# Kernel optimization log

Hardware: AMD Instinct MI355X
Metric: run time of the kernel (lower is better)

The kernel has to match this reference:

```python
import jax, jax.numpy as jnp
import numpy as np

N_NODES = 50000
N_EDGES = 800000
IN_DIM = 128
HID = 128
NUM_CLASSES = 2


def setup_inputs() -> dict:
    key = jax.random.key(0)
    ks = jax.random.split(key, 16)
    inp = {
        "adj_row": jax.random.randint(ks[0], (N_EDGES,), 0, N_NODES),
        "adj_col": jax.random.randint(ks[1], (N_EDGES,), 0, N_NODES),
        "adj_vals": jax.random.uniform(ks[2], (N_EDGES,), dtype=jnp.float32),
        "input_feature": jax.random.normal(ks[3], (N_NODES, IN_DIM), dtype=jnp.float32),
        "graph_indicator": jax.random.randint(ks[4], (N_NODES,), 0, 64),
        # GCN layer params (kaiming-uniform-ish init; zeros bias like the torch module)
        "W1": jax.random.uniform(ks[5], (IN_DIM, HID), jnp.float32, -1, 1) * np.sqrt(6.0 / IN_DIM),
        "b1": jnp.zeros((HID,), jnp.float32),
        "W2": jax.random.uniform(ks[6], (HID, HID), jnp.float32, -1, 1) * np.sqrt(6.0 / HID),
        "b2": jnp.zeros((HID,), jnp.float32),
        "W3": jax.random.uniform(ks[7], (HID, HID), jnp.float32, -1, 1) * np.sqrt(6.0 / HID),
        "b3": jnp.zeros((HID,), jnp.float32),
        # fc params (torch.nn.Linear default init range)
        "fcW1": jax.random.uniform(ks[8], (3 * HID, HID), jnp.float32, -1, 1) / np.sqrt(3 * HID),
        "fcb1": jax.random.uniform(ks[9], (HID,), jnp.float32, -1, 1) / np.sqrt(3 * HID),
        "fcW2": jax.random.uniform(ks[10], (HID, HID // 2), jnp.float32, -1, 1) / np.sqrt(HID),
        "fcb2": jax.random.uniform(ks[11], (HID // 2,), jnp.float32, -1, 1) / np.sqrt(HID),
        "fcW3": jax.random.uniform(ks[12], (HID // 2, NUM_CLASSES), jnp.float32, -1, 1) / np.sqrt(HID // 2),
        "fcb3": jax.random.uniform(ks[13], (NUM_CLASSES,), jnp.float32, -1, 1) / np.sqrt(HID // 2),
    }
    return inp


def _gcn_layer(row, col, vals, x, W, b, n_nodes):
    # support = X @ W  -> dense GEMM
    support = x @ W
    # sparse.mm(A, support): out[i] = sum_{e: row[e]=i} vals[e] * support[col[e]]
    msgs = support[col] * vals[:, None]  # [E, D] gather + scale
    agg = jax.ops.segment_sum(msgs, row, num_segments=n_nodes)
    return agg + b


def reference(adj_row, adj_col, adj_vals, input_feature, graph_indicator,
              W1, b1, W2, b2, W3, b3, fcW1, fcb1, fcW2, fcb2, fcW3, fcb3):
    n = input_feature.shape[0]
    g1 = jax.nn.relu(_gcn_layer(adj_row, adj_col, adj_vals, input_feature, W1, b1, n))
    g2 = jax.nn.relu(_gcn_layer(adj_row, adj_col, adj_vals, g1, W2, b2, n))
    g3 = jax.nn.relu(_gcn_layer(adj_row, adj_col, adj_vals, g2, W3, b3, n))
    feat = jnp.concatenate([g1, g2, g3], axis=1)  # [N, 3*HID]
    h = jax.nn.relu(feat @ fcW1 + fcb1)
    h = jax.nn.relu(h @ fcW2 + fcb2)
    logits = h @ fcW3 + fcb3
    return logits
```

## Files before the change

kernel.cpp:

```cpp
#include <hip/hip_runtime.h>
#include <hip/hip_bf16.h>

#define N_NODES 50000
#define N_EDGES 800000
#define NBK 391
#define BCAP 2560

static inline int cdiv(int a, int b) { return (a + b - 1) / b; }

typedef __attribute__((ext_vector_type(8))) short short8;
typedef __attribute__((ext_vector_type(4))) float f32x4;

__device__ __forceinline__ float b2f(unsigned short u) {
    union { unsigned int i; float f; } c;
    c.i = ((unsigned int)u) << 16;
    return c.f;
}
__device__ __forceinline__ unsigned short f2bb(float f) {
    __hip_bfloat16 h = __float2bfloat16(f);
    return *(unsigned short*)&h;
}


__global__ __launch_bounds__(256)
void binA_kernel(const int* __restrict__ row, const int* __restrict__ col,
                 const float* __restrict__ vals, int* __restrict__ bcursor,
                 int2* __restrict__ tmp, int E) {
    __shared__ int hist[NBK];
    __shared__ int base[NBK];
    const int CH = 4096;
    int e0 = blockIdx.x * CH;
    for (int i = threadIdx.x; i < NBK; i += 256) hist[i] = 0;
    __syncthreads();
    for (int i = threadIdx.x; i < CH; i += 256) {
        int e = e0 + i;
        if (e < E) atomicAdd(&hist[row[e] >> 7], 1);
    }
    __syncthreads();
    for (int i = threadIdx.x; i < NBK; i += 256) {
        int c = hist[i];
        base[i] = (c > 0) ? atomicAdd(&bcursor[i], c) : 0;
        hist[i] = 0;
    }
    __syncthreads();
    for (int i = threadIdx.x; i < CH; i += 256) {
        int e = e0 + i;
        if (e < E) {
            int r = row[e];
            int b = r >> 7;
            int rk = atomicAdd(&hist[b], 1);
            tmp[base[b] + rk] = make_int2(((r & 127) << 16) | col[e],
                                          __float_as_int(vals[e]));
        }
    }
}

__global__ __launch_bounds__(512)
void bscan_kernel(const int* __restrict__ bcursor, int* __restrict__ bbase) {
    __shared__ int s[512];
    int t = threadIdx.x;
    int v = (t < NBK) ? (bcursor[t] - t * BCAP) : 0;
    s[t] = v;
    __syncthreads();
    for (int off = 1; off < 512; off <<= 1) {
        int u = (t >= off) ? s[t - off] : 0;
        __syncthreads();
        s[t] += u;
        __syncthreads();
    }
    if (t < NBK) bbase[t] = s[t] - v;
    if (t == NBK - 1) bbase[NBK] = s[t];
}

__global__ __launch_bounds__(256)
void binB_kernel(const int2* __restrict__ tmp, const int* __restrict__ bcursor,
                 const int* __restrict__ bbase, int* __restrict__ row_ptr,
                 int2* __restrict__ epack, int N) {
    int b = blockIdx.x;
    int r0 = b << 7;
    int nr = N - r0; if (nr > 128) nr = 128;
    __shared__ int cnt[128];
    __shared__ int cur[128];
    int t = threadIdx.x;
    if (t < 128) cnt[t] = 0;
    __syncthreads();
    int slab = b * BCAP;
    int send = bcursor[b];
    int obase = bbase[b];
    for (int i = slab + t; i < send; i += 256)
        atomicAdd(&cnt[tmp[i].x >> 16], 1);
    __syncthreads();
    if (t < 128) cur[t] = cnt[t];
    __syncthreads();
    for (int off = 1; off < 128; off <<= 1) {
        int u = (t >= off && t < 128) ? cur[t - off] : 0;
        __syncthreads();
        if (t < 128) cur[t] += u;
        __syncthreads();
    }
    if (t < 128) {
        int ex = cur[t] - cnt[t];
        int pos = obase + ex;
        cur[t] = pos;
        if (t < nr) row_ptr[r0 + t] = pos;
    }
    if (b == NBK - 1 && t == 128) row_ptr[N] = bbase[NBK];
    __syncthreads();
    for (int i = slab + t; i < send; i += 256) {
        int2 v = tmp[i];
        int rl = v.x >> 16;
        int c = v.x & 0xffff;
        int pos = atomicAdd(&cur[rl], 1);
        epack[pos] = make_int2(c, v.y);
    }
}


__device__ __forceinline__ void pack_one(const float* __restrict__ W,
                                         __hip_bfloat16* __restrict__ out,
                                         int K, int N, int t) {
    int lane = t & 63;
    int kc = (t >> 6) % (K / 32);
    int nt = (t >> 6) / (K / 32);
    int kbase = kc * 32 + (lane >> 4) * 8;
    int col = nt * 16 + (lane & 15);
    __hip_bfloat16* dst = out + (size_t)t * 8;
#pragma unroll
    for (int j = 0; j < 8; ++j)
        dst[j] = __float2bfloat16(W[(size_t)(kbase + j) * N + col]);
}

__global__ __launch_bounds__(256)
void prep_kernel(const float* __restrict__ W1, const float* __restrict__ W2,
                 const float* __restrict__ W3, const float* __restrict__ fcW1,
                 const float* __restrict__ fcW2,
                 __hip_bfloat16* __restrict__ pW1, __hip_bfloat16* __restrict__ pW2,
                 __hip_bfloat16* __restrict__ pW3, __hip_bfloat16* __restrict__ pfcW1,
                 __hip_bfloat16* __restrict__ pfcW2, int* __restrict__ bcursor) {
    int b = blockIdx.x;
    if (b < 8)       pack_one(W1,  pW1,  128, 128, b * 256 + threadIdx.x);
    else if (b < 16) pack_one(W2,  pW2,  128, 128, (b - 8) * 256 + threadIdx.x);
    else if (b < 24) pack_one(W3,  pW3,  128, 128, (b - 16) * 256 + threadIdx.x);
    else if (b < 48) pack_one(fcW1, pfcW1, 384, 128, (b - 24) * 256 + threadIdx.x);
    else if (b < 52) pack_one(fcW2, pfcW2, 128, 64, (b - 48) * 256 + threadIdx.x);
    else {
        int t = (b - 52) * 256 + threadIdx.x;
        if (t < NBK) bcursor[t] = t * BCAP;
    }
}

template <int KTOT, int N, bool RELU, bool BIAS, bool AFP32>
__global__ __launch_bounds__(256, 3)
void mfma_gemm(const void* __restrict__ Aptr, int lda,
               const __hip_bfloat16* __restrict__ pW,
               const float* __restrict__ bias,
               __hip_bfloat16* __restrict__ C, int ldc, int M) {
    constexpr int NS = (N == 128) ? 2 : 1;
    constexpr int KC = KTOT / 32;
    __shared__ unsigned short As[64][136];
    const int tid = threadIdx.x;
    const int wave = tid >> 6;
    const int lane = tid & 63;
    const int ln15 = lane & 15;
    const int quad = lane >> 4;
    const int m0 = blockIdx.x * 64;
    const int ntw = wave * NS;

    f32x4 acc[4][NS];
#pragma unroll
    for (int s = 0; s < 4; ++s)
#pragma unroll
        for (int h = 0; h < NS; ++h) acc[s][h] = (f32x4){0.f, 0.f, 0.f, 0.f};

    for (int kb = 0; kb < KTOT / 128; ++kb) {
#pragma unroll
        for (int i = 0; i < 4; ++i) {
            int idx = tid + i * 256;
            int r = idx >> 4;
            int c8 = (idx & 15) * 8;
            if constexpr (AFP32) {
                const float* A = (const float*)Aptr;
                uint4 pk = {0, 0, 0, 0};
                if (m0 + r < M) {
                    const float* src = &A[(size_t)(m0 + r) * lda + kb * 128 + c8];
                    float4 a = *(const float4*)src;
                    float4 bq = *(const float4*)(src + 4);
                    pk.x = f2bb(a.x) | ((unsigned int)f2bb(a.y) << 16);
                    pk.y = f2bb(a.z) | ((unsigned int)f2bb(a.w) << 16);
                    pk.z = f2bb(bq.x) | ((unsigned int)f2bb(bq.y) << 16);
                    pk.w = f2bb(bq.z) | ((unsigned int)f2bb(bq.w) << 16);
                }
                *(uint4*)&As[r][c8] = pk;
            } else {
                const __hip_bfloat16* A = (const __hip_bfloat16*)Aptr;
                uint4 v = *(const uint4*)&A[(size_t)(m0 + r) * lda + kb * 128 + c8];
                *(uint4*)&As[r][c8] = v;
            }
        }
        __syncthreads();
#pragma unroll
        for (int kc = 0; kc < 4; ++kc) {
            short8 af[4];
#pragma unroll
            for (int s = 0; s < 4; ++s)
                af[s] = *(const short8*)&As[s * 16 + ln15][kc * 32 + quad * 8];
            short8 bf[NS];
#pragma unroll
            for (int h = 0; h < NS; ++h) {
                int kcg = kb * 4 + kc;
                bf[h] = *(const short8*)&pW[((size_t)((ntw + h) * KC + kcg) * 64 + lane) * 8];
            }
#pragma unroll
            for (int s = 0; s < 4; ++s)
#pragma unroll
                for (int h = 0; h < NS; ++h)
                    acc[s][h] = __builtin_amdgcn_mfma_f32_16x16x32_bf16(
                        af[s], bf[h], acc[s][h], 0, 0, 0);
        }
        __syncthreads();
    }

#pragma unroll
    for (int s = 0; s < 4; ++s) {
#pragma unroll
        for (int h = 0; h < NS; ++h) {
            int col = (ntw + h) * 16 + ln15;
            float bv = BIAS ? bias[col] : 0.f;
#pragma unroll
            for (int r = 0; r < 4; ++r) {
                int row = m0 + s * 16 + quad * 4 + r;
                if (row < M) {
                    float v = acc[s][h][r] + bv;
                    if (RELU) v = fmaxf(v, 0.f);
                    C[(size_t)row * ldc + col] = __float2bfloat16(v);
                }
            }
        }
    }
}

__global__ __launch_bounds__(256, 3)
void fc123_kernel(const __hip_bfloat16* __restrict__ featb,
                  const __hip_bfloat16* __restrict__ pfcW1,
                  const float* __restrict__ fcb1,
                  const __hip_bfloat16* __restrict__ pfcW2,
                  const float* __restrict__ fcb2,
                  const float* __restrict__ fcW3, const float* __restrict__ fcb3,
                  float* __restrict__ out, int M) {
    __shared__ unsigned short As[64][136];
    __shared__ float w3s[128];
    __shared__ float b3s[2];
    const int tid = threadIdx.x;
    const int wave = tid >> 6;
    const int lane = tid & 63;
    const int ln15 = lane & 15;
    const int quad = lane >> 4;
    const int m0 = blockIdx.x * 64;
    if (tid < 128) w3s[tid] = fcW3[tid];
    if (tid < 2) b3s[tid] = fcb3[tid];

    f32x4 acc[4][2];
#pragma unroll
    for (int s = 0; s < 4; ++s)
#pragma unroll
        for (int h = 0; h < 2; ++h) acc[s][h] = (f32x4){0.f, 0.f, 0.f, 0.f};
    for (int kb = 0; kb < 3; ++kb) {
#pragma unroll
        for (int i = 0; i < 4; ++i) {
            int idx = tid + i * 256;
            int r = idx >> 4;
            int c8 = (idx & 15) * 8;
            uint4 v = *(const uint4*)&featb[(size_t)(m0 + r) * 384 + kb * 128 + c8];
            *(uint4*)&As[r][c8] = v;
        }
        __syncthreads();
#pragma unroll
        for (int kc = 0; kc < 4; ++kc) {
            short8 af[4];
#pragma unroll
            for (int s = 0; s < 4; ++s)
                af[s] = *(const short8*)&As[s * 16 + ln15][kc * 32 + quad * 8];
            short8 bf[2];
#pragma unroll
            for (int h = 0; h < 2; ++h) {
                int kcg = kb * 4 + kc;
                bf[h] = *(const short8*)&pfcW1[((size_t)((wave * 2 + h) * 12 + kcg) * 64 + lane) * 8];
            }
#pragma unroll
            for (int s = 0; s < 4; ++s)
#pragma unroll
                for (int h = 0; h < 2; ++h)
                    acc[s][h] = __builtin_amdgcn_mfma_f32_16x16x32_bf16(
                        af[s], bf[h], acc[s][h], 0, 0, 0);
        }
        __syncthreads();
    }
#pragma unroll
    for (int s = 0; s < 4; ++s)
#pragma unroll
        for (int h = 0; h < 2; ++h) {
            int col = (wave * 2 + h) * 16 + ln15;
            float bv = fcb1[col];
#pragma unroll
            for (int r = 0; r < 4; ++r) {
                int row = s * 16 + quad * 4 + r;
                As[row][col] = f2bb(fmaxf(acc[s][h][r] + bv, 0.f));
            }
        }
    __syncthreads();

    f32x4 acc2[4];
#pragma unroll
    for (int s = 0; s < 4; ++s) acc2[s] = (f32x4){0.f, 0.f, 0.f, 0.f};
#pragma unroll
    for (int kc = 0; kc < 4; ++kc) {
        short8 af[4];
#pragma unroll
        for (int s = 0; s < 4; ++s)
            af[s] = *(const short8*)&As[s * 16 + ln15][kc * 32 + quad * 8];
        short8 bfw = *(const short8*)&pfcW2[((size_t)(wave * 4 + kc) * 64 + lane) * 8];
#pragma unroll
        for (int s = 0; s < 4; ++s)
            acc2[s] = __builtin_amdgcn_mfma_f32_16x16x32_bf16(af[s], bfw, acc2[s], 0, 0, 0);
    }
    __syncthreads();
    {
        int col2 = wave * 16 + ln15;
        float bv = fcb2[col2];
#pragma unroll
        for (int s = 0; s < 4; ++s)
#pragma unroll
            for (int r = 0; r < 4; ++r) {
                int row = s * 16 + quad * 4 + r;
                As[row][col2] = f2bb(fmaxf(acc2[s][r] + bv, 0.f));
            }
    }
    __syncthreads();

    if (tid < 128) {
        int row = tid >> 1, cls = tid & 1;
        int grow = m0 + row;
        if (grow < M) {
            float a = b3s[cls];
#pragma unroll
            for (int k = 0; k < 64; ++k)
                a += b2f(As[row][k]) * w3s[k * 2 + cls];
            out[(size_t)grow * 2 + cls] = a;
        }
    }
}

__global__ __launch_bounds__(256)
void spmm_kernel(const int* __restrict__ row_ptr, const int2* __restrict__ epack,
                 const __hip_bfloat16* __restrict__ support,
                 const float* __restrict__ bias, __hip_bfloat16* __restrict__ out,
                 int ldo, int n) {
    int wv = threadIdx.x >> 6;
    int l = threadIdx.x & 63;
    int node = blockIdx.x * 4 + wv;
    if (node >= n) return;
    int start = row_ptr[node], end = row_ptr[node + 1];
    float ax = 0.f, ay = 0.f;
    int p = start;
    for (; p + 4 <= end; p += 4) {
        int2 e0 = epack[p], e1 = epack[p + 1], e2 = epack[p + 2], e3 = epack[p + 3];
        ushort2 u0 = *(const ushort2*)&support[(size_t)e0.x * 128 + l * 2];
        ushort2 u1 = *(const ushort2*)&support[(size_t)e1.x * 128 + l * 2];
        ushort2 u2 = *(const ushort2*)&support[(size_t)e2.x * 128 + l * 2];
        ushort2 u3 = *(const ushort2*)&support[(size_t)e3.x * 128 + l * 2];
        float v0 = __int_as_float(e0.y), v1 = __int_as_float(e1.y);
        float v2 = __int_as_float(e2.y), v3 = __int_as_float(e3.y);
        ax += v0 * b2f(u0.x) + v1 * b2f(u1.x) + v2 * b2f(u2.x) + v3 * b2f(u3.x);
        ay += v0 * b2f(u0.y) + v1 * b2f(u1.y) + v2 * b2f(u2.y) + v3 * b2f(u3.y);
    }
    for (; p < end; ++p) {
        int2 e0 = epack[p];
        float v0 = __int_as_float(e0.y);
        ushort2 u0 = *(const ushort2*)&support[(size_t)e0.x * 128 + l * 2];
        ax += v0 * b2f(u0.x);
        ay += v0 * b2f(u0.y);
    }
    ushort2 ov;
    ov.x = f2bb(fmaxf(ax + bias[l * 2 + 0], 0.f));
    ov.y = f2bb(fmaxf(ay + bias[l * 2 + 1], 0.f));
    *(ushort2*)&out[(size_t)node * ldo + l * 2] = ov;
}

extern "C" void kernel_launch(void* const* d_in, const int* in_sizes, int n_in,
                              void* d_out, int out_size, void* d_ws, size_t ws_size,
                              hipStream_t stream) {
    const int*   adj_row  = (const int*)d_in[0];
    const int*   adj_col  = (const int*)d_in[1];
    const float* adj_vals = (const float*)d_in[2];
    const float* x        = (const float*)d_in[3];
    const float* W1   = (const float*)d_in[5];
    const float* b1   = (const float*)d_in[6];
    const float* W2   = (const float*)d_in[7];
    const float* b2   = (const float*)d_in[8];
    const float* W3   = (const float*)d_in[9];
    const float* b3   = (const float*)d_in[10];
    const float* fcW1 = (const float*)d_in[11];
    const float* fcb1 = (const float*)d_in[12];
    const float* fcW2 = (const float*)d_in[13];
    const float* fcb2 = (const float*)d_in[14];
    const float* fcW3 = (const float*)d_in[15];
    const float* fcb3 = (const float*)d_in[16];
    float* out = (float*)d_out;

    const int N = N_NODES, E = N_EDGES;
    const int Mpad = 50048;

    char* p = (char*)d_ws;
    auto alloc = [&](size_t bytes) {
        char* q = p;
        p += (bytes + 255) & ~(size_t)255;
        return q;
    };
    __hip_bfloat16* featb    = (__hip_bfloat16*)alloc((size_t)Mpad * 384 * 2);
    __hip_bfloat16* supportb = (__hip_bfloat16*)alloc((size_t)Mpad * 128 * 2);
    __hip_bfloat16* pW1   = (__hip_bfloat16*)alloc(16384 * 2);
    __hip_bfloat16* pW2   = (__hip_bfloat16*)alloc(16384 * 2);
    __hip_bfloat16* pW3   = (__hip_bfloat16*)alloc(16384 * 2);
    __hip_bfloat16* pfcW1 = (__hip_bfloat16*)alloc(49152 * 2);
    __hip_bfloat16* pfcW2 = (__hip_bfloat16*)alloc(8192 * 2);
    int*   row_ptr   = (int*)alloc((size_t)(N + 1) * 4);
    int*   bbase     = (int*)alloc((size_t)(NBK + 1) * 4);
    int*   bcursor   = (int*)alloc((size_t)NBK * 4);
    int2*  epack     = (int2*)alloc((size_t)E * 8);
    int2*  tmp = (int2*)(featb + (size_t)Mpad * 384 - (size_t)NBK * BCAP * 4);

    prep_kernel<<<54, 256, 0, stream>>>(W1, W2, W3, fcW1, fcW2,
                                        pW1, pW2, pW3, pfcW1, pfcW2, bcursor);
    binA_kernel<<<cdiv(E, 4096), 256, 0, stream>>>(adj_row, adj_col, adj_vals,
                                                   bcursor, tmp, E);
    bscan_kernel<<<1, 512, 0, stream>>>(bcursor, bbase);
    binB_kernel<<<NBK, 256, 0, stream>>>(tmp, bcursor, bbase, row_ptr, epack, N);

    const int gemmGrid = cdiv(N, 64);
    const int spmmGrid = cdiv(N, 4);

    mfma_gemm<128, 128, false, false, true><<<gemmGrid, 256, 0, stream>>>(
        x, 128, pW1, nullptr, supportb, 128, N);
    spmm_kernel<<<spmmGrid, 256, 0, stream>>>(row_ptr, epack, supportb, b1,
                                              featb + 0, 384, N);
    mfma_gemm<128, 128, false, false, false><<<gemmGrid, 256, 0, stream>>>(
        featb + 0, 384, pW2, nullptr, supportb, 128, N);
    spmm_kernel<<<spmmGrid, 256, 0, stream>>>(row_ptr, epack, supportb, b2,
                                              featb + 128, 384, N);
    mfma_gemm<128, 128, false, false, false><<<gemmGrid, 256, 0, stream>>>(
        featb + 128, 384, pW3, nullptr, supportb, 128, N);
    spmm_kernel<<<spmmGrid, 256, 0, stream>>>(row_ptr, epack, supportb, b3,
                                              featb + 256, 384, N);

    fc123_kernel<<<gemmGrid, 256, 0, stream>>>(featb, pfcW1, fcb1, pfcW2, fcb2,
                                               fcW3, fcb3, out, N);
}
```

Baseline: 302.6 us.

## Fuse SpMM aggregation with following GEMM and final FC into combined kernels

Each sparse aggregation is now done inside a 64-node block, written straight to shared memory and immediately multiplied by the next layer weight, so the separate GEMM kernels and their reloads of the feature matrix go away. The last layer's aggregation feeds fcW1 directly, so g3 is never written to global memory and the feature buffer shrinks to 256 columns. Support buffers are double-buffered and the edge list is read with nontemporal loads. The cost is that one block now aggregates 64 nodes with four waves instead of many small blocks, which lowers gather parallelism and latency hiding per block.

```diff
diff --git a/kernel.cpp b/kernel.cpp
--- a/kernel.cpp
+++ b/kernel.cpp
@@ -149,14 +149,10 @@
     }
 }
 
-template <int KTOT, int N, bool RELU, bool BIAS, bool AFP32>
 __global__ __launch_bounds__(256, 3)
-void mfma_gemm(const void* __restrict__ Aptr, int lda,
-               const __hip_bfloat16* __restrict__ pW,
-               const float* __restrict__ bias,
-               __hip_bfloat16* __restrict__ C, int ldc, int M) {
-    constexpr int NS = (N == 128) ? 2 : 1;
-    constexpr int KC = KTOT / 32;
+void gemm1_kernel(const float* __restrict__ A,
+                  const __hip_bfloat16* __restrict__ pW,
+                  __hip_bfloat16* __restrict__ C, int M) {
     __shared__ unsigned short As[64][136];
     const int tid = threadIdx.x;
     const int wave = tid >> 6;
@@ -164,90 +160,179 @@
     const int ln15 = lane & 15;
     const int quad = lane >> 4;
     const int m0 = blockIdx.x * 64;
-    const int ntw = wave * NS;
-
-    f32x4 acc[4][NS];
+    const int ntw = wave * 2;
+
+    f32x4 acc[4][2];
 #pragma unroll
     for (int s = 0; s < 4; ++s)
 #pragma unroll
-        for (int h = 0; h < NS; ++h) acc[s][h] = (f32x4){0.f, 0.f, 0.f, 0.f};
-
-    for (int kb = 0; kb < KTOT / 128; ++kb) {
-#pragma unroll
-        for (int i = 0; i < 4; ++i) {
-            int idx = tid + i * 256;
-            int r = idx >> 4;
-            int c8 = (idx & 15) * 8;
-            if constexpr (AFP32) {
-                const float* A = (const float*)Aptr;
-                uint4 pk = {0, 0, 0, 0};
-                if (m0 + r < M) {
-                    const float* src = &A[(size_t)(m0 + r) * lda + kb * 128 + c8];
-                    float4 a = *(const float4*)src;
-                    float4 bq = *(const float4*)(src + 4);
-                    pk.x = f2bb(a.x) | ((unsigned int)f2bb(a.y) << 16);
-                    pk.y = f2bb(a.z) | ((unsigned int)f2bb(a.w) << 16);
-                    pk.z = f2bb(bq.x) | ((unsigned int)f2bb(bq.y) << 16);
-                    pk.w = f2bb(bq.z) | ((unsigned int)f2bb(bq.w) << 16);
-                }
-                *(uint4*)&As[r][c8] = pk;
-            } else {
-                const __hip_bfloat16* A = (const __hip_bfloat16*)Aptr;
-                uint4 v = *(const uint4*)&A[(size_t)(m0 + r) * lda + kb * 128 + c8];
-                *(uint4*)&As[r][c8] = v;
-            }
-        }
-        __syncthreads();
-#pragma unroll
-        for (int kc = 0; kc < 4; ++kc) {
-            short8 af[4];
-#pragma unroll
-            for (int s = 0; s < 4; ++s)
-                af[s] = *(const short8*)&As[s * 16 + ln15][kc * 32 + quad * 8];
-            short8 bf[NS];
-#pragma unroll
-            for (int h = 0; h < NS; ++h) {
-                int kcg = kb * 4 + kc;
-                bf[h] = *(const short8*)&pW[((size_t)((ntw + h) * KC + kcg) * 64 + lane) * 8];
-            }
-#pragma unroll
-            for (int s = 0; s < 4; ++s)
-#pragma unroll
-                for (int h = 0; h < NS; ++h)
-                    acc[s][h] = __builtin_amdgcn_mfma_f32_16x16x32_bf16(
-                        af[s], bf[h], acc[s][h], 0, 0, 0);
-        }
-        __syncthreads();
-    }
-
-#pragma unroll
-    for (int s = 0; s < 4; ++s) {
-#pragma unroll
-        for (int h = 0; h < NS; ++h) {
+        for (int h = 0; h < 2; ++h) acc[s][h] = (f32x4){0.f, 0.f, 0.f, 0.f};
+
+#pragma unroll
+    for (int i = 0; i < 4; ++i) {
+        int idx = tid + i * 256;
+        int r = idx >> 4;
+        int c8 = (idx & 15) * 8;
+        uint4 pk = {0, 0, 0, 0};
+        if (m0 + r < M) {
+            const float* src = &A[(size_t)(m0 + r) * 128 + c8];
+            float4 a = *(const float4*)src;
+            float4 bq = *(const float4*)(src + 4);
+            pk.x = f2bb(a.x) | ((unsigned int)f2bb(a.y) << 16);
+            pk.y = f2bb(a.z) | ((unsigned int)f2bb(a.w) << 16);
+            pk.z = f2bb(bq.x) | ((unsigned int)f2bb(bq.y) << 16);
+            pk.w = f2bb(bq.z) | ((unsigned int)f2bb(bq.w) << 16);
+        }
+        *(uint4*)&As[r][c8] = pk;
+    }
+    __syncthreads();
+#pragma unroll
+    for (int kc = 0; kc < 4; ++kc) {
+        short8 af[4];
+#pragma unroll
+        for (int s = 0; s < 4; ++s)
+            af[s] = *(const short8*)&As[s * 16 + ln15][kc * 32 + quad * 8];
+        short8 bf[2];
+#pragma unroll
+        for (int h = 0; h < 2; ++h)
+            bf[h] = *(const short8*)&pW[((size_t)((ntw + h) * 4 + kc) * 64 + lane) * 8];
+#pragma unroll
+        for (int s = 0; s < 4; ++s)
+#pragma unroll
+            for (int h = 0; h < 2; ++h)
+                acc[s][h] = __builtin_amdgcn_mfma_f32_16x16x32_bf16(
+                    af[s], bf[h], acc[s][h], 0, 0, 0);
+    }
+
+#pragma unroll
+    for (int s = 0; s < 4; ++s)
+#pragma unroll
+        for (int h = 0; h < 2; ++h) {
             int col = (ntw + h) * 16 + ln15;
-            float bv = BIAS ? bias[col] : 0.f;
 #pragma unroll
             for (int r = 0; r < 4; ++r) {
                 int row = m0 + s * 16 + quad * 4 + r;
-                if (row < M) {
-                    float v = acc[s][h][r] + bv;
-                    if (RELU) v = fmaxf(v, 0.f);
-                    C[(size_t)row * ldc + col] = __float2bfloat16(v);
-                }
+                if (row < M)
+                    C[(size_t)row * 128 + col] = __float2bfloat16(acc[s][h][r]);
             }
         }
+}
+
+__device__ __forceinline__ void agg_node(const int* __restrict__ row_ptr,
+                                         const long long* __restrict__ ep,
+                                         const __hip_bfloat16* __restrict__ support,
+                                         int node, int lane, float& ax, float& ay) {
+    int pstart = row_ptr[node], pend = row_ptr[node + 1];
+    int p = pstart;
+    for (; p + 4 <= pend; p += 4) {
+        long long v0 = __builtin_nontemporal_load(&ep[p]);
+        long long v1 = __builtin_nontemporal_load(&ep[p + 1]);
+        long long v2 = __builtin_nontemporal_load(&ep[p + 2]);
+        long long v3 = __builtin_nontemporal_load(&ep[p + 3]);
+        ushort2 u0 = *(const ushort2*)&support[(size_t)(unsigned int)(v0 & 0xffffffff) * 128 + lane * 2];
+        ushort2 u1 = *(const ushort2*)&support[(size_t)(unsigned int)(v1 & 0xffffffff) * 128 + lane * 2];
+        ushort2 u2 = *(const ushort2*)&support[(size_t)(unsigned int)(v2 & 0xffffffff) * 128 + lane * 2];
+        ushort2 u3 = *(const ushort2*)&support[(size_t)(unsigned int)(v3 & 0xffffffff) * 128 + lane * 2];
+        float f0 = __int_as_float((int)(v0 >> 32));
+        float f1 = __int_as_float((int)(v1 >> 32));
+        float f2 = __int_as_float((int)(v2 >> 32));
+        float f3 = __int_as_float((int)(v3 >> 32));
+        ax += f0 * b2f(u0.x) + f1 * b2f(u1.x) + f2 * b2f(u2.x) + f3 * b2f(u3.x);
+        ay += f0 * b2f(u0.y) + f1 * b2f(u1.y) + f2 * b2f(u2.y) + f3 * b2f(u3.y);
+    }
+    for (; p < pend; ++p) {
+        long long v0 = __builtin_nontemporal_load(&ep[p]);
+        ushort2 u0 = *(const ushort2*)&support[(size_t)(unsigned int)(v0 & 0xffffffff) * 128 + lane * 2];
+        float f0 = __int_as_float((int)(v0 >> 32));
+        ax += f0 * b2f(u0.x);
+        ay += f0 * b2f(u0.y);
     }
 }
 
 __global__ __launch_bounds__(256, 3)
-void fc123_kernel(const __hip_bfloat16* __restrict__ featb,
-                  const __hip_bfloat16* __restrict__ pfcW1,
-                  const float* __restrict__ fcb1,
-                  const __hip_bfloat16* __restrict__ pfcW2,
-                  const float* __restrict__ fcb2,
-                  const float* __restrict__ fcW3, const float* __restrict__ fcb3,
-                  float* __restrict__ out, int M) {
+void spmm_gemm_kernel(const int* __restrict__ row_ptr, const int2* __restrict__ epack,
+                      const __hip_bfloat16* __restrict__ support_in,
+                      const float* __restrict__ bias,
+                      __hip_bfloat16* __restrict__ featb_slice,
+                      const __hip_bfloat16* __restrict__ pW,
+                      __hip_bfloat16* __restrict__ support_out, int M) {
     __shared__ unsigned short As[64][136];
+    const int tid = threadIdx.x;
+    const int wave = tid >> 6;
+    const int lane = tid & 63;
+    const int ln15 = lane & 15;
+    const int quad = lane >> 4;
+    const int m0 = blockIdx.x * 64;
+    const long long* ep = (const long long*)epack;
+    const float b0 = bias[lane * 2], b1v = bias[lane * 2 + 1];
+
+    for (int i = 0; i < 16; ++i) {
+        int r = wave * 16 + i;
+        int node = m0 + r;
+        float ax = 0.f, ay = 0.f;
+        unsigned int packed = 0;
+        if (node < M) {
+            agg_node(row_ptr, ep, support_in, node, lane, ax, ay);
+            ax = fmaxf(ax + b0, 0.f);
+            ay = fmaxf(ay + b1v, 0.f);
+            packed = (unsigned int)f2bb(ax) | ((unsigned int)f2bb(ay) << 16);
+            __builtin_nontemporal_store(packed,
+                (unsigned int*)&featb_slice[(size_t)node * 256 + lane * 2]);
+        }
+        *(unsigned int*)&As[r][lane * 2] = packed;
+    }
+    __syncthreads();
+
+    f32x4 acc[4][2];
+#pragma unroll
+    for (int s = 0; s < 4; ++s)
+#pragma unroll
+        for (int h = 0; h < 2; ++h) acc[s][h] = (f32x4){0.f, 0.f, 0.f, 0.f};
+#pragma unroll
+    for (int kc = 0; kc < 4; ++kc) {
+        short8 af[4];
+#pragma unroll
+        for (int s = 0; s < 4; ++s)
+            af[s] = *(const short8*)&As[s * 16 + ln15][kc * 32 + quad * 8];
+        short8 bf[2];
+#pragma unroll
+        for (int h = 0; h < 2; ++h)
+            bf[h] = *(const short8*)&pW[((size_t)((wave * 2 + h) * 4 + kc) * 64 + lane) * 8];
+#pragma unroll
+        for (int s = 0; s < 4; ++s)
+#pragma unroll
+            for (int h = 0; h < 2; ++h)
+                acc[s][h] = __builtin_amdgcn_mfma_f32_16x16x32_bf16(
+                    af[s], bf[h], acc[s][h], 0, 0, 0);
+    }
+
+#pragma unroll
+    for (int s = 0; s < 4; ++s)
+#pragma unroll
+        for (int h = 0; h < 2; ++h) {
+            int col = (wave * 2 + h) * 16 + ln15;
+#pragma unroll
+            for (int r = 0; r < 4; ++r) {
+                int row = m0 + s * 16 + quad * 4 + r;
+                if (row < M)
+                    support_out[(size_t)row * 128 + col] = __float2bfloat16(acc[s][h][r]);
+            }
+        }
+}
+
+__global__ __launch_bounds__(256, 3)
+void spmm_fc_kernel(const int* __restrict__ row_ptr, const int2* __restrict__ epack,
+                    const __hip_bfloat16* __restrict__ support_in,
+                    const float* __restrict__ bias3,
+                    const __hip_bfloat16* __restrict__ featb,
+                    const __hip_bfloat16* __restrict__ pfcW1,
+                    const float* __restrict__ fcb1,
+                    const __hip_bfloat16* __restrict__ pfcW2,
+                    const float* __restrict__ fcb2,
+                    const float* __restrict__ fcW3, const float* __restrict__ fcb3,
+                    float* __restrict__ out, int M) {
+    __shared__ unsigned short As[64][136];
+    __shared__ unsigned short Bs[64][136];
     __shared__ float w3s[128];
     __shared__ float b3s[2];
     const int tid = threadIdx.x;
@@ -256,21 +341,40 @@
     const int ln15 = lane & 15;
     const int quad = lane >> 4;
     const int m0 = blockIdx.x * 64;
+    const long long* ep = (const long long*)epack;
     if (tid < 128) w3s[tid] = fcW3[tid];
     if (tid < 2) b3s[tid] = fcb3[tid];
+    const float b0 = bias3[lane * 2], b1v = bias3[lane * 2 + 1];
+
+    for (int i = 0; i < 16; ++i) {
+        int r = wave * 16 + i;
+        int node = m0 + r;
+        float ax = 0.f, ay = 0.f;
+        unsigned int packed = 0;
+        if (node < M) {
+            agg_node(row_ptr, ep, support_in, node, lane, ax, ay);
+            ax = fmaxf(ax + b0, 0.f);
+            ay = fmaxf(ay + b1v, 0.f);
+            packed = (unsigned int)f2bb(ax) | ((unsigned int)f2bb(ay) << 16);
+        }
+        *(unsigned int*)&Bs[r][lane * 2] = packed;
+    }
+    __syncthreads();
 
     f32x4 acc[4][2];
 #pragma unroll
     for (int s = 0; s < 4; ++s)
 #pragma unroll
         for (int h = 0; h < 2; ++h) acc[s][h] = (f32x4){0.f, 0.f, 0.f, 0.f};
-    for (int kb = 0; kb < 3; ++kb) {
+    for (int kb = 0; kb < 2; ++kb) {
 #pragma unroll
         for (int i = 0; i < 4; ++i) {
             int idx = tid + i * 256;
             int r = idx >> 4;
             int c8 = (idx & 15) * 8;
-            uint4 v = *(const uint4*)&featb[(size_t)(m0 + r) * 384 + kb * 128 + c8];
+            uint4 v = {0, 0, 0, 0};
+            if (m0 + r < M)
+                v = *(const uint4*)&featb[(size_t)(m0 + r) * 256 + kb * 128 + c8];
             *(uint4*)&As[r][c8] = v;
         }
         __syncthreads();
@@ -295,6 +399,26 @@
         }
         __syncthreads();
     }
+#pragma unroll
+    for (int kc = 0; kc < 4; ++kc) {
+        short8 af[4];
+#pragma unroll
+        for (int s = 0; s < 4; ++s)
+            af[s] = *(const short8*)&Bs[s * 16 + ln15][kc * 32 + quad * 8];
+        short8 bf[2];
+#pragma unroll
+        for (int h = 0; h < 2; ++h) {
+            int kcg = 8 + kc;
+            bf[h] = *(const short8*)&pfcW1[((size_t)((wave * 2 + h) * 12 + kcg) * 64 + lane) * 8];
+        }
+#pragma unroll
+        for (int s = 0; s < 4; ++s)
+#pragma unroll
+            for (int h = 0; h < 2; ++h)
+                acc[s][h] = __builtin_amdgcn_mfma_f32_16x16x32_bf16(
+                    af[s], bf[h], acc[s][h], 0, 0, 0);
+    }
+    __syncthreads();
 #pragma unroll
     for (int s = 0; s < 4; ++s)
 #pragma unroll
@@ -348,42 +472,6 @@
             out[(size_t)grow * 2 + cls] = a;
         }
     }
-}
-
-__global__ __launch_bounds__(256)
-void spmm_kernel(const int* __restrict__ row_ptr, const int2* __restrict__ epack,
-                 const __hip_bfloat16* __restrict__ support,
-                 const float* __restrict__ bias, __hip_bfloat16* __restrict__ out,
-                 int ldo, int n) {
-    int wv = threadIdx.x >> 6;
-    int l = threadIdx.x & 63;
-    int node = blockIdx.x * 4 + wv;
-    if (node >= n) return;
-    int start = row_ptr[node], end = row_ptr[node + 1];
-    float ax = 0.f, ay = 0.f;
-    int p = start;
-    for (; p + 4 <= end; p += 4) {
-        int2 e0 = epack[p], e1 = epack[p + 1], e2 = epack[p + 2], e3 = epack[p + 3];
-        ushort2 u0 = *(const ushort2*)&support[(size_t)e0.x * 128 + l * 2];
-        ushort2 u1 = *(const ushort2*)&support[(size_t)e1.x * 128 + l * 2];
-        ushort2 u2 = *(const ushort2*)&support[(size_t)e2.x * 128 + l * 2];
-        ushort2 u3 = *(const ushort2*)&support[(size_t)e3.x * 128 + l * 2];
-        float v0 = __int_as_float(e0.y), v1 = __int_as_float(e1.y);
-        float v2 = __int_as_float(e2.y), v3 = __int_as_float(e3.y);
-        ax += v0 * b2f(u0.x) + v1 * b2f(u1.x) + v2 * b2f(u2.x) + v3 * b2f(u3.x);
-        ay += v0 * b2f(u0.y) + v1 * b2f(u1.y) + v2 * b2f(u2.y) + v3 * b2f(u3.y);
-    }
-    for (; p < end; ++p) {
-        int2 e0 = epack[p];
-        float v0 = __int_as_float(e0.y);
-        ushort2 u0 = *(const ushort2*)&support[(size_t)e0.x * 128 + l * 2];
-        ax += v0 * b2f(u0.x);
-        ay += v0 * b2f(u0.y);
-    }
-    ushort2 ov;
-    ov.x = f2bb(fmaxf(ax + bias[l * 2 + 0], 0.f));
-    ov.y = f2bb(fmaxf(ay + bias[l * 2 + 1], 0.f));
-    *(ushort2*)&out[(size_t)node * ldo + l * 2] = ov;
 }
 
 extern "C" void kernel_launch(void* const* d_in, const int* in_sizes, int n_in,
@@ -416,8 +504,9 @@
         p += (bytes + 255) & ~(size_t)255;
         return q;
     };
-    __hip_bfloat16* featb    = (__hip_bfloat16*)alloc((size_t)Mpad * 384 * 2);
-    __hip_bfloat16* supportb = (__hip_bfloat16*)alloc((size_t)Mpad * 128 * 2);
+    __hip_bfloat16* featb    = (__hip_bfloat16*)alloc((size_t)Mpad * 256 * 2);
+    __hip_bfloat16* supportA = (__hip_bfloat16*)alloc((size_t)Mpad * 128 * 2);
+    __hip_bfloat16* supportB = (__hip_bfloat16*)alloc((size_t)Mpad * 128 * 2);
     __hip_bfloat16* pW1   = (__hip_bfloat16*)alloc(16384 * 2);
     __hip_bfloat16* pW2   = (__hip_bfloat16*)alloc(16384 * 2);
     __hip_bfloat16* pW3   = (__hip_bfloat16*)alloc(16384 * 2);
@@ -427,7 +516,7 @@
     int*   bbase     = (int*)alloc((size_t)(NBK + 1) * 4);
     int*   bcursor   = (int*)alloc((size_t)NBK * 4);
     int2*  epack     = (int2*)alloc((size_t)E * 8);
-    int2*  tmp = (int2*)(featb + (size_t)Mpad * 384 - (size_t)NBK * BCAP * 4);
+    int2*  tmp       = (int2*)alloc((size_t)NBK * BCAP * 8);
 
     prep_kernel<<<54, 256, 0, stream>>>(W1, W2, W3, fcW1, fcW2,
                                         pW1, pW2, pW3, pfcW1, pfcW2, bcursor);
@@ -436,22 +525,14 @@
     bscan_kernel<<<1, 512, 0, stream>>>(bcursor, bbase);
     binB_kernel<<<NBK, 256, 0, stream>>>(tmp, bcursor, bbase, row_ptr, epack, N);
 
-    const int gemmGrid = cdiv(N, 64);
-    const int spmmGrid = cdiv(N, 4);
-
-    mfma_gemm<128, 128, false, false, true><<<gemmGrid, 256, 0, stream>>>(
-        x, 128, pW1, nullptr, supportb, 128, N);
-    spmm_kernel<<<spmmGrid, 256, 0, stream>>>(row_ptr, epack, supportb, b1,
-                                              featb + 0, 384, N);
-    mfma_gemm<128, 128, false, false, false><<<gemmGrid, 256, 0, stream>>>(
-        featb + 0, 384, pW2, nullptr, supportb, 128, N);
-    spmm_kernel<<<spmmGrid, 256, 0, stream>>>(row_ptr, epack, supportb, b2,
-                                              featb + 128, 384, N);
-    mfma_gemm<128, 128, false, false, false><<<gemmGrid, 256, 0, stream>>>(
-        featb + 128, 384, pW3, nullptr, supportb, 128, N);
-    spmm_kernel<<<spmmGrid, 256, 0, stream>>>(row_ptr, epack, supportb, b3,
-                                              featb + 256, 384, N);
-
-    fc123_kernel<<<gemmGrid, 256, 0, stream>>>(featb, pfcW1, fcb1, pfcW2, fcb2,
-                                               fcW3, fcb3, out, N);
-}
+    const int grid = cdiv(N, 64);
+
+    gemm1_kernel<<<grid, 256, 0, stream>>>(x, pW1, supportA, N);
+    spmm_gemm_kernel<<<grid, 256, 0, stream>>>(row_ptr, epack, supportA, b1,
+                                               featb + 0, pW2, supportB, N);
+    spmm_gemm_kernel<<<grid, 256, 0, stream>>>(row_ptr, epack, supportB, b2,
+                                               featb + 128, pW3, supportA, N);
+    spmm_fc_kernel<<<grid, 256, 0, stream>>>(row_ptr, epack, supportA, b3,
+                                             featb, pfcW1, fcb1, pfcW2, fcb2,
+                                             fcW3, fcb3, out, N);
+}
```

Result: slower. 410.9 us (+35.8%).

## Fuse edge binning, first GEMM and weight packing into one heterogeneous launch

Applied to the files above, without the earlier changes.

Merges the edge-binning pass, the layer-1 X@W1 GEMM (with W1 converted to bf16 fragments in registers) and the packing of the other weights into a single kernel whose blocks pick a role from their block index. This removes the prep kernel and the separate first GEMM launch, and lets the binning and the GEMM run side by side on the device. The bin cursors become relative offsets cleared with a memset, and the temporary edge buffer gets its own allocation instead of aliasing the feature buffer. The SpMM edge loads become nontemporal 64-bit loads and the output stores become nontemporal stores. The GEMM template is specialised to K=128 with no bias. The fused kernel needs more shared memory per block, which may lower the number of resident blocks.

```diff
diff --git a/kernel.cpp b/kernel.cpp
--- a/kernel.cpp
+++ b/kernel.cpp
@@ -21,45 +21,148 @@
     return *(unsigned short*)&h;
 }
 
+__device__ __forceinline__ void pack_one(const float* __restrict__ W,
+                                         __hip_bfloat16* __restrict__ out,
+                                         int K, int N, int t) {
+    int lane = t & 63;
+    int kc = (t >> 6) % (K / 32);
+    int nt = (t >> 6) / (K / 32);
+    int kbase = kc * 32 + (lane >> 4) * 8;
+    int col = nt * 16 + (lane & 15);
+    __hip_bfloat16* dst = out + (size_t)t * 8;
+#pragma unroll
+    for (int j = 0; j < 8; ++j)
+        dst[j] = __float2bfloat16(W[(size_t)(kbase + j) * N + col]);
+}
 
 __global__ __launch_bounds__(256)
-void binA_kernel(const int* __restrict__ row, const int* __restrict__ col,
-                 const float* __restrict__ vals, int* __restrict__ bcursor,
-                 int2* __restrict__ tmp, int E) {
+void stage1_kernel(const int* __restrict__ row, const int* __restrict__ col,
+                   const float* __restrict__ vals, int* __restrict__ bcursor,
+                   int2* __restrict__ tmp, int E,
+                   const float* __restrict__ x, __hip_bfloat16* __restrict__ support,
+                   int M,
+                   const float* __restrict__ W1, const float* __restrict__ W2,
+                   const float* __restrict__ W3, const float* __restrict__ fcW1,
+                   const float* __restrict__ fcW2,
+                   __hip_bfloat16* __restrict__ pW2, __hip_bfloat16* __restrict__ pW3,
+                   __hip_bfloat16* __restrict__ pfcW1, __hip_bfloat16* __restrict__ pfcW2) {
+    __shared__ unsigned short As[64][136];
     __shared__ int hist[NBK];
     __shared__ int base[NBK];
-    const int CH = 4096;
-    int e0 = blockIdx.x * CH;
-    for (int i = threadIdx.x; i < NBK; i += 256) hist[i] = 0;
-    __syncthreads();
-    for (int i = threadIdx.x; i < CH; i += 256) {
-        int e = e0 + i;
-        if (e < E) atomicAdd(&hist[row[e] >> 7], 1);
-    }
-    __syncthreads();
-    for (int i = threadIdx.x; i < NBK; i += 256) {
-        int c = hist[i];
-        base[i] = (c > 0) ? atomicAdd(&bcursor[i], c) : 0;
-        hist[i] = 0;
-    }
-    __syncthreads();
-    for (int i = threadIdx.x; i < CH; i += 256) {
-        int e = e0 + i;
-        if (e < E) {
-            int r = row[e];
-            int b = r >> 7;
-            int rk = atomicAdd(&hist[b], 1);
-            tmp[base[b] + rk] = make_int2(((r & 127) << 16) | col[e],
-                                          __float_as_int(vals[e]));
-        }
-    }
-}
+    const int b = blockIdx.x;
+    const int tid = threadIdx.x;
+
+    if (b < 196) {
+        const int CH = 4096;
+        int e0 = b * CH;
+        for (int i = tid; i < NBK; i += 256) hist[i] = 0;
+        __syncthreads();
+        for (int i = tid; i < CH; i += 256) {
+            int e = e0 + i;
+            if (e < E) atomicAdd(&hist[row[e] >> 7], 1);
+        }
+        __syncthreads();
+        for (int i = tid; i < NBK; i += 256) {
+            int c = hist[i];
+            base[i] = (c > 0) ? (i * BCAP + atomicAdd(&bcursor[i], c)) : 0;
+            hist[i] = 0;
+        }
+        __syncthreads();
+        for (int i = tid; i < CH; i += 256) {
+            int e = e0 + i;
+            if (e < E) {
+                int r = row[e];
+                int bk = r >> 7;
+                int rk = atomicAdd(&hist[bk], 1);
+                tmp[base[bk] + rk] = make_int2(((r & 127) << 16) | col[e],
+                                               __float_as_int(vals[e]));
+            }
+        }
+        return;
+    }
+
+    if (b < 978) {
+        const int wave = tid >> 6;
+        const int lane = tid & 63;
+        const int ln15 = lane & 15;
+        const int quad = lane >> 4;
+        const int m0 = (b - 196) * 64;
+
+        short8 bfr[4][2];
+#pragma unroll
+        for (int kc = 0; kc < 4; ++kc)
+#pragma unroll
+            for (int h = 0; h < 2; ++h)
+#pragma unroll
+                for (int j = 0; j < 8; ++j)
+                    bfr[kc][h][j] = (short)f2bb(
+                        W1[(size_t)(kc * 32 + quad * 8 + j) * 128 + (wave * 2 + h) * 16 + ln15]);
+
+#pragma unroll
+        for (int i = 0; i < 4; ++i) {
+            int idx = tid + i * 256;
+            int r = idx >> 4;
+            int c8 = (idx & 15) * 8;
+            uint4 pk = {0, 0, 0, 0};
+            if (m0 + r < M) {
+                const float* src = &x[(size_t)(m0 + r) * 128 + c8];
+                float4 a = *(const float4*)src;
+                float4 bq = *(const float4*)(src + 4);
+                pk.x = f2bb(a.x) | ((unsigned int)f2bb(a.y) << 16);
+                pk.y = f2bb(a.z) | ((unsigned int)f2bb(a.w) << 16);
+                pk.z = f2bb(bq.x) | ((unsigned int)f2bb(bq.y) << 16);
+                pk.w = f2bb(bq.z) | ((unsigned int)f2bb(bq.w) << 16);
+            }
+            *(uint4*)&As[r][c8] = pk;
+        }
+        __syncthreads();
+
+        f32x4 acc[4][2];
+#pragma unroll
+        for (int s = 0; s < 4; ++s)
+#pragma unroll
+            for (int h = 0; h < 2; ++h) acc[s][h] = (f32x4){0.f, 0.f, 0.f, 0.f};
+#pragma unroll
+        for (int kc = 0; kc < 4; ++kc) {
+            short8 af[4];
+#pragma unroll
+            for (int s = 0; s < 4; ++s)
+                af[s] = *(const short8*)&As[s * 16 + ln15][kc * 32 + quad * 8];
+#pragma unroll
+            for (int s = 0; s < 4; ++s)
+#pragma unroll
+                for (int h = 0; h < 2; ++h)
+                    acc[s][h] = __builtin_amdgcn_mfma_f32_16x16x32_bf16(
+                        af[s], bfr[kc][h], acc[s][h], 0, 0, 0);
+        }
+#pragma unroll
+        for (int s = 0; s < 4; ++s)
+#pragma unroll
+            for (int h = 0; h < 2; ++h) {
+                int cl = (wave * 2 + h) * 16 + ln15;
+#pragma unroll
+                for (int r = 0; r < 4; ++r) {
+                    int rw = m0 + s * 16 + quad * 4 + r;
+                    if (rw < M)
+                        support[(size_t)rw * 128 + cl] = __float2bfloat16(acc[s][h][r]);
+                }
+            }
+        return;
+    }
+
+    int pb = b - 978;
+    if (pb < 8)       pack_one(W2,  pW2,  128, 128, pb * 256 + tid);
+    else if (pb < 16) pack_one(W3,  pW3,  128, 128, (pb - 8) * 256 + tid);
+    else if (pb < 40) pack_one(fcW1, pfcW1, 384, 128, (pb - 16) * 256 + tid);
+    else              pack_one(fcW2, pfcW2, 128, 64, (pb - 40) * 256 + tid);
+}
+
 
 __global__ __launch_bounds__(512)
 void bscan_kernel(const int* __restrict__ bcursor, int* __restrict__ bbase) {
     __shared__ int s[512];
     int t = threadIdx.x;
-    int v = (t < NBK) ? (bcursor[t] - t * BCAP) : 0;
+    int v = (t < NBK) ? bcursor[t] : 0;
     s[t] = v;
     __syncthreads();
     for (int off = 1; off < 512; off <<= 1) {
@@ -85,7 +188,7 @@
     if (t < 128) cnt[t] = 0;
     __syncthreads();
     int slab = b * BCAP;
-    int send = bcursor[b];
+    int send = slab + bcursor[b];
     int obase = bbase[b];
     for (int i = slab + t; i < send; i += 256)
         atomicAdd(&cnt[tmp[i].x >> 16], 1);
@@ -115,48 +218,10 @@
     }
 }
 
-
-__device__ __forceinline__ void pack_one(const float* __restrict__ W,
-                                         __hip_bfloat16* __restrict__ out,
-                                         int K, int N, int t) {
-    int lane = t & 63;
-    int kc = (t >> 6) % (K / 32);
-    int nt = (t >> 6) / (K / 32);
-    int kbase = kc * 32 + (lane >> 4) * 8;
-    int col = nt * 16 + (lane & 15);
-    __hip_bfloat16* dst = out + (size_t)t * 8;
-#pragma unroll
-    for (int j = 0; j < 8; ++j)
-        dst[j] = __float2bfloat16(W[(size_t)(kbase + j) * N + col]);
-}
-
-__global__ __launch_bounds__(256)
-void prep_kernel(const float* __restrict__ W1, const float* __restrict__ W2,
-                 const float* __restrict__ W3, const float* __restrict__ fcW1,
-                 const float* __restrict__ fcW2,
-                 __hip_bfloat16* __restrict__ pW1, __hip_bfloat16* __restrict__ pW2,
-                 __hip_bfloat16* __restrict__ pW3, __hip_bfloat16* __restrict__ pfcW1,
-                 __hip_bfloat16* __restrict__ pfcW2, int* __restrict__ bcursor) {
-    int b = blockIdx.x;
-    if (b < 8)       pack_one(W1,  pW1,  128, 128, b * 256 + threadIdx.x);
-    else if (b < 16) pack_one(W2,  pW2,  128, 128, (b - 8) * 256 + threadIdx.x);
-    else if (b < 24) pack_one(W3,  pW3,  128, 128, (b - 16) * 256 + threadIdx.x);
-    else if (b < 48) pack_one(fcW1, pfcW1, 384, 128, (b - 24) * 256 + threadIdx.x);
-    else if (b < 52) pack_one(fcW2, pfcW2, 128, 64, (b - 48) * 256 + threadIdx.x);
-    else {
-        int t = (b - 52) * 256 + threadIdx.x;
-        if (t < NBK) bcursor[t] = t * BCAP;
-    }
-}
-
-template <int KTOT, int N, bool RELU, bool BIAS, bool AFP32>
 __global__ __launch_bounds__(256, 3)
-void mfma_gemm(const void* __restrict__ Aptr, int lda,
+void mfma_gemm(const __hip_bfloat16* __restrict__ A, int lda,
                const __hip_bfloat16* __restrict__ pW,
-               const float* __restrict__ bias,
-               __hip_bfloat16* __restrict__ C, int ldc, int M) {
-    constexpr int NS = (N == 128) ? 2 : 1;
-    constexpr int KC = KTOT / 32;
+               __hip_bfloat16* __restrict__ C, int M) {
     __shared__ unsigned short As[64][136];
     const int tid = threadIdx.x;
     const int wave = tid >> 6;
@@ -164,79 +229,94 @@
     const int ln15 = lane & 15;
     const int quad = lane >> 4;
     const int m0 = blockIdx.x * 64;
-    const int ntw = wave * NS;
-
-    f32x4 acc[4][NS];
+    const int ntw = wave * 2;
+
+    f32x4 acc[4][2];
 #pragma unroll
     for (int s = 0; s < 4; ++s)
 #pragma unroll
-        for (int h = 0; h < NS; ++h) acc[s][h] = (f32x4){0.f, 0.f, 0.f, 0.f};
-
-    for (int kb = 0; kb < KTOT / 128; ++kb) {
-#pragma unroll
-        for (int i = 0; i < 4; ++i) {
-            int idx = tid + i * 256;
-            int r = idx >> 4;
-            int c8 = (idx & 15) * 8;
-            if constexpr (AFP32) {
-                const float* A = (const float*)Aptr;
-                uint4 pk = {0, 0, 0, 0};
-                if (m0 + r < M) {
-                    const float* src = &A[(size_t)(m0 + r) * lda + kb * 128 + c8];
-                    float4 a = *(const float4*)src;
-                    float4 bq = *(const float4*)(src + 4);
-                    pk.x = f2bb(a.x) | ((unsigned int)f2bb(a.y) << 16);
-                    pk.y = f2bb(a.z) | ((unsigned int)f2bb(a.w) << 16);
-                    pk.z = f2bb(bq.x) | ((unsigned int)f2bb(bq.y) << 16);
-                    pk.w = f2bb(bq.z) | ((unsigned int)f2bb(bq.w) << 16);
-                }
-                *(uint4*)&As[r][c8] = pk;
-            } else {
-                const __hip_bfloat16* A = (const __hip_bfloat16*)Aptr;
-                uint4 v = *(const uint4*)&A[(size_t)(m0 + r) * lda + kb * 128 + c8];
-                *(uint4*)&As[r][c8] = v;
-            }
-        }
-        __syncthreads();
-#pragma unroll
-        for (int kc = 0; kc < 4; ++kc) {
-            short8 af[4];
-#pragma unroll
-            for (int s = 0; s < 4; ++s)
-                af[s] = *(const short8*)&As[s * 16 + ln15][kc * 32 + quad * 8];
-            short8 bf[NS];
-#pragma unroll
-            for (int h = 0; h < NS; ++h) {
-                int kcg = kb * 4 + kc;
-                bf[h] = *(const short8*)&pW[((size_t)((ntw + h) * KC + kcg) * 64 + lane) * 8];
-            }
-#pragma unroll
-            for (int s = 0; s < 4; ++s)
-#pragma unroll
-                for (int h = 0; h < NS; ++h)
-                    acc[s][h] = __builtin_amdgcn_mfma_f32_16x16x32_bf16(
-                        af[s], bf[h], acc[s][h], 0, 0, 0);
-        }
-        __syncthreads();
-    }
-
-#pragma unroll
-    for (int s = 0; s < 4; ++s) {
-#pragma unroll
-        for (int h = 0; h < NS; ++h) {
-            int col = (ntw + h) * 16 + ln15;
-            float bv = BIAS ? bias[col] : 0.f;
+        for (int h = 0; h < 2; ++h) acc[s][h] = (f32x4){0.f, 0.f, 0.f, 0.f};
+
+#pragma unroll
+    for (int i = 0; i < 4; ++i) {
+        int idx = tid + i * 256;
+        int r = idx >> 4;
+        int c8 = (idx & 15) * 8;
+        uint4 v = *(const uint4*)&A[(size_t)(m0 + r) * lda + c8];
+        *(uint4*)&As[r][c8] = v;
+    }
+    __syncthreads();
+#pragma unroll
+    for (int kc = 0; kc < 4; ++kc) {
+        short8 af[4];
+#pragma unroll
+        for (int s = 0; s < 4; ++s)
+            af[s] = *(const short8*)&As[s * 16 + ln15][kc * 32 + quad * 8];
+        short8 bf[2];
+#pragma unroll
+        for (int h = 0; h < 2; ++h)
+            bf[h] = *(const short8*)&pW[((size_t)((ntw + h) * 4 + kc) * 64 + lane) * 8];
+#pragma unroll
+        for (int s = 0; s < 4; ++s)
+#pragma unroll
+            for (int h = 0; h < 2; ++h)
+                acc[s][h] = __builtin_amdgcn_mfma_f32_16x16x32_bf16(
+                    af[s], bf[h], acc[s][h], 0, 0, 0);
+    }
+
+#pragma unroll
+    for (int s = 0; s < 4; ++s)
+#pragma unroll
+        for (int h = 0; h < 2; ++h) {
+            int cl = (ntw + h) * 16 + ln15;
 #pragma unroll
             for (int r = 0; r < 4; ++r) {
-                int row = m0 + s * 16 + quad * 4 + r;
-                if (row < M) {
-                    float v = acc[s][h][r] + bv;
-                    if (RELU) v = fmaxf(v, 0.f);
-                    C[(size_t)row * ldc + col] = __float2bfloat16(v);
-                }
-            }
-        }
-    }
+                int rw = m0 + s * 16 + quad * 4 + r;
+                if (rw < M)
+                    C[(size_t)rw * 128 + cl] = __float2bfloat16(acc[s][h][r]);
+            }
+        }
+}
+
+__global__ __launch_bounds__(256)
+void spmm_kernel(const int* __restrict__ row_ptr, const int2* __restrict__ epack,
+                 const __hip_bfloat16* __restrict__ support,
+                 const float* __restrict__ bias, __hip_bfloat16* __restrict__ out,
+                 int ldo, int n) {
+    int wv = threadIdx.x >> 6;
+    int l = threadIdx.x & 63;
+    int node = blockIdx.x * 4 + wv;
+    if (node >= n) return;
+    const long long* ep = (const long long*)epack;
+    int start = row_ptr[node], end = row_ptr[node + 1];
+    float ax = 0.f, ay = 0.f;
+    int p = start;
+    for (; p + 4 <= end; p += 4) {
+        long long v0 = __builtin_nontemporal_load(&ep[p]);
+        long long v1 = __builtin_nontemporal_load(&ep[p + 1]);
+        long long v2 = __builtin_nontemporal_load(&ep[p + 2]);
+        long long v3 = __builtin_nontemporal_load(&ep[p + 3]);
+        ushort2 u0 = *(const ushort2*)&support[(size_t)(unsigned int)(v0 & 0xffffffff) * 128 + l * 2];
+        ushort2 u1 = *(const ushort2*)&support[(size_t)(unsigned int)(v1 & 0xffffffff) * 128 + l * 2];
+        ushort2 u2 = *(const ushort2*)&support[(size_t)(unsigned int)(v2 & 0xffffffff) * 128 + l * 2];
+        ushort2 u3 = *(const ushort2*)&support[(size_t)(unsigned int)(v3 & 0xffffffff) * 128 + l * 2];
+        float f0 = __int_as_float((int)(v0 >> 32));
+        float f1 = __int_as_float((int)(v1 >> 32));
+        float f2 = __int_as_float((int)(v2 >> 32));
+        float f3 = __int_as_float((int)(v3 >> 32));
+        ax += f0 * b2f(u0.x) + f1 * b2f(u1.x) + f2 * b2f(u2.x) + f3 * b2f(u3.x);
+        ay += f0 * b2f(u0.y) + f1 * b2f(u1.y) + f2 * b2f(u2.y) + f3 * b2f(u3.y);
+    }
+    for (; p < end; ++p) {
+        long long v0 = __builtin_nontemporal_load(&ep[p]);
+        ushort2 u0 = *(const ushort2*)&support[(size_t)(unsigned int)(v0 & 0xffffffff) * 128 + l * 2];
+        float f0 = __int_as_float((int)(v0 >> 32));
+        ax += f0 * b2f(u0.x);
+        ay += f0 * b2f(u0.y);
+    }
+    unsigned int packed = (unsigned int)f2bb(fmaxf(ax + bias[l * 2 + 0], 0.f))
+                        | ((unsigned int)f2bb(fmaxf(ay + bias[l * 2 + 1], 0.f)) << 16);
+    __builtin_nontemporal_store(packed, (unsigned int*)&out[(size_t)node * ldo + l * 2]);
 }
 
 __global__ __launch_bounds__(256, 3)
@@ -348,42 +428,6 @@
             out[(size_t)grow * 2 + cls] = a;
         }
     }
-}
-
-__global__ __launch_bounds__(256)
-void spmm_kernel(const int* __restrict__ row_ptr, const int2* __restrict__ epack,
-                 const __hip_bfloat16* __restrict__ support,
-                 const float* __restrict__ bias, __hip_bfloat16* __restrict__ out,
-                 int ldo, int n) {
-    int wv = threadIdx.x >> 6;
-    int l = threadIdx.x & 63;
-    int node = blockIdx.x * 4 + wv;
-    if (node >= n) return;
-    int start = row_ptr[node], end = row_ptr[node + 1];
-    float ax = 0.f, ay = 0.f;
-    int p = start;
-    for (; p + 4 <= end; p += 4) {
-        int2 e0 = epack[p], e1 = epack[p + 1], e2 = epack[p + 2], e3 = epack[p + 3];
-        ushort2 u0 = *(const ushort2*)&support[(size_t)e0.x * 128 + l * 2];
-        ushort2 u1 = *(const ushort2*)&support[(size_t)e1.x * 128 + l * 2];
-        ushort2 u2 = *(const ushort2*)&support[(size_t)e2.x * 128 + l * 2];
-        ushort2 u3 = *(const ushort2*)&support[(size_t)e3.x * 128 + l * 2];
-        float v0 = __int_as_float(e0.y), v1 = __int_as_float(e1.y);
-        float v2 = __int_as_float(e2.y), v3 = __int_as_float(e3.y);
-        ax += v0 * b2f(u0.x) + v1 * b2f(u1.x) + v2 * b2f(u2.x) + v3 * b2f(u3.x);
-        ay += v0 * b2f(u0.y) + v1 * b2f(u1.y) + v2 * b2f(u2.y) + v3 * b2f(u3.y);
-    }
-    for (; p < end; ++p) {
-        int2 e0 = epack[p];
-        float v0 = __int_as_float(e0.y);
-        ushort2 u0 = *(const ushort2*)&support[(size_t)e0.x * 128 + l * 2];
-        ax += v0 * b2f(u0.x);
-        ay += v0 * b2f(u0.y);
-    }
-    ushort2 ov;
-    ov.x = f2bb(fmaxf(ax + bias[l * 2 + 0], 0.f));
-    ov.y = f2bb(fmaxf(ay + bias[l * 2 + 1], 0.f));
-    *(ushort2*)&out[(size_t)node * ldo + l * 2] = ov;
 }
 
 extern "C" void kernel_launch(void* const* d_in, const int* in_sizes, int n_in,
@@ -418,7 +462,6 @@
     };
     __hip_bfloat16* featb    = (__hip_bfloat16*)alloc((size_t)Mpad * 384 * 2);
     __hip_bfloat16* supportb = (__hip_bfloat16*)alloc((size_t)Mpad * 128 * 2);
-    __hip_bfloat16* pW1   = (__hip_bfloat16*)alloc(16384 * 2);
     __hip_bfloat16* pW2   = (__hip_bfloat16*)alloc(16384 * 2);
     __hip_bfloat16* pW3   = (__hip_bfloat16*)alloc(16384 * 2);
     __hip_bfloat16* pfcW1 = (__hip_bfloat16*)alloc(49152 * 2);
@@ -427,28 +470,25 @@
     int*   bbase     = (int*)alloc((size_t)(NBK + 1) * 4);
     int*   bcursor   = (int*)alloc((size_t)NBK * 4);
     int2*  epack     = (int2*)alloc((size_t)E * 8);
-    int2*  tmp = (int2*)(featb + (size_t)Mpad * 384 - (size_t)NBK * BCAP * 4);
-
-    prep_kernel<<<54, 256, 0, stream>>>(W1, W2, W3, fcW1, fcW2,
-                                        pW1, pW2, pW3, pfcW1, pfcW2, bcursor);
-    binA_kernel<<<cdiv(E, 4096), 256, 0, stream>>>(adj_row, adj_col, adj_vals,
-                                                   bcursor, tmp, E);
+    int2*  tmp       = (int2*)alloc((size_t)NBK * BCAP * 8);
+
+    hipMemsetAsync(bcursor, 0, (size_t)NBK * 4, stream);
+    stage1_kernel<<<1022, 256, 0, stream>>>(adj_row, adj_col, adj_vals, bcursor, tmp, E,
+                                            x, supportb, N,
+                                            W1, W2, W3, fcW1, fcW2,
+                                            pW2, pW3, pfcW1, pfcW2);
     bscan_kernel<<<1, 512, 0, stream>>>(bcursor, bbase);
     binB_kernel<<<NBK, 256, 0, stream>>>(tmp, bcursor, bbase, row_ptr, epack, N);
 
     const int gemmGrid = cdiv(N, 64);
     const int spmmGrid = cdiv(N, 4);
 
-    mfma_gemm<128, 128, false, false, true><<<gemmGrid, 256, 0, stream>>>(
-        x, 128, pW1, nullptr, supportb, 128, N);
     spmm_kernel<<<spmmGrid, 256, 0, stream>>>(row_ptr, epack, supportb, b1,
                                               featb + 0, 384, N);
-    mfma_gemm<128, 128, false, false, false><<<gemmGrid, 256, 0, stream>>>(
-        featb + 0, 384, pW2, nullptr, supportb, 128, N);
+    mfma_gemm<<<gemmGrid, 256, 0, stream>>>(featb + 0, 384, pW2, supportb, N);
     spmm_kernel<<<spmmGrid, 256, 0, stream>>>(row_ptr, epack, supportb, b2,
                                               featb + 128, 384, N);
-    mfma_gemm<128, 128, false, false, false><<<gemmGrid, 256, 0, stream>>>(
-        featb + 128, 384, pW3, nullptr, supportb, 128, N);
+    mfma_gemm<<<gemmGrid, 256, 0, stream>>>(featb + 128, 384, pW3, supportb, N);
     spmm_kernel<<<spmmGrid, 256, 0, stream>>>(row_ptr, epack, supportb, b3,
                                               featb + 256, 384, N);
 
```

Measured after the change: 329.3 us. +8.8%, slower.
